# Optimization experiments

Hardware: AMD Instinct MI355X
Metric: run time of the kernel (lower is better)

## Reference

```python
import jax, jax.numpy as jnp
import numpy as np

B, L, E, N, H = 64, 128, 512, 512, 1024


def setup_inputs() -> dict:
    key = jax.random.key(0)
    ks = jax.random.split(key, 16)
    s = 0.02
    return {
        "embeddings": jax.random.normal(ks[0], (B, L, E), jnp.float32),
        "value": jax.random.normal(ks[1], (B, N, H), jnp.float32),
        "value_mask": jnp.ones((B, N), jnp.float32),
        "state": jax.random.normal(ks[2], (B, H), jnp.float32),
        # GRUCell params (PyTorch layout: gates ordered r, z, n)
        "W_ih": jax.random.normal(ks[3], (3 * H, E + H), jnp.float32) * s,
        "b_ih": jnp.zeros((3 * H,), jnp.float32),
        "W_hh": jax.random.normal(ks[4], (3 * H, H), jnp.float32) * s,
        "b_hh": jnp.zeros((3 * H,), jnp.float32),
        # MLP (additive/Bahdanau) attention params
        "Wq": jax.random.normal(ks[5], (H, H), jnp.float32) * s,
        "Wk": jax.random.normal(ks[6], (H, H), jnp.float32) * s,
        "v_att": jax.random.normal(ks[7], (H,), jnp.float32) * s,
        # hidden_mlp: Linear(2H -> H)
        "Wm": jax.random.normal(ks[8], (H, 2 * H), jnp.float32) * s,
        "bm": jnp.zeros((H,), jnp.float32),
    }


def reference(embeddings, value, value_mask, state, W_ih, b_ih, W_hh, b_hh, Wq, Wk, v_att, Wm, bm):
    # Precompute attention keys once: B x N x H
    keys = jnp.einsum('bnh,kh->bnk', value, Wk)
    neg = jnp.float32(-1e9)

    def step(h, emb_t):
        # GRU cell (PyTorch semantics)
        x = jnp.concatenate([emb_t, h], axis=-1)          # B x (E+H)
        gx = x @ W_ih.T + b_ih                            # B x 3H
        gh = h @ W_hh.T + b_hh                            # B x 3H
        xr, xz, xn = jnp.split(gx, 3, axis=-1)
        hr, hz, hn = jnp.split(gh, 3, axis=-1)
        r = jax.nn.sigmoid(xr + hr)
        z = jax.nn.sigmoid(xz + hz)
        n = jnp.tanh(xn + r * hn)
        rnn_out = (1.0 - z) * n + z * h                   # B x H
        # Additive attention
        q = rnn_out @ Wq.T                                # B x H
        score = jnp.einsum('bnh,h->bn', jnp.tanh(q[:, None, :] + keys), v_att)
        score = jnp.where(value_mask > 0, score, neg)
        attn = jax.nn.softmax(score, axis=-1)             # B x N
        context = jnp.einsum('bn,bnh->bh', attn, value)   # B x H
        # hidden MLP + tanh (dropout = identity in eval mode)
        new_state = jnp.tanh(jnp.concatenate([rnn_out, context], axis=-1) @ Wm.T + bm)
        return new_state, (new_state, attn)

    emb_t_first = jnp.swapaxes(embeddings, 0, 1)          # L x B x E
    _, (outs, attns) = jax.lax.scan(step, state, emb_t_first)
    outputs = jnp.swapaxes(outs, 0, 1)                    # B x L x H
    attns = jnp.swapaxes(attns, 0, 1)                     # B x L x N
    return outputs, attns
```

## Files before the change

### kernel.cpp

```cpp
#include <hip/hip_runtime.h>
#include <hip/hip_bf16.h>

typedef __bf16 bf16;
typedef __bf16 bf16x8 __attribute__((ext_vector_type(8)));
typedef __bf16 bf16x4 __attribute__((ext_vector_type(4)));
typedef float floatx4 __attribute__((ext_vector_type(4)));

#define MFMA16(a, b, c) __builtin_amdgcn_mfma_f32_16x16x32_bf16((a), (b), (c), 0, 0, 0)

static constexpr int Bd = 64, Ld = 128, Ed = 512, Nd = 512, Hd = 1024;
static constexpr float LOG2E = 1.4426950408889634f;
static constexpr float TWO_LOG2E = 2.8853900817779268f;

__device__ __forceinline__ float fexp2(float x) { return __builtin_amdgcn_exp2f(x); }
__device__ __forceinline__ float frcp(float x) { return __builtin_amdgcn_rcpf(x); }
__device__ __forceinline__ float sigmoid_f(float x) { return frcp(1.0f + fexp2(-x * LOG2E)); }
__device__ __forceinline__ float tanh_f(float x) { return 1.0f - 2.0f * frcp(fexp2(x * TWO_LOG2E) + 1.0f); }

__device__ __forceinline__ bf16x8 cvt8(const float* p) {
    float4 f0 = *(const float4*)p;
    float4 f1 = *(const float4*)(p + 4);
    bf16x8 r = {(bf16)f0.x, (bf16)f0.y, (bf16)f0.z, (bf16)f0.w,
                (bf16)f1.x, (bf16)f1.y, (bf16)f1.z, (bf16)f1.w};
    return r;
}

__global__ __launch_bounds__(256) void k_conv(const float* __restrict__ src, bf16* __restrict__ dst, int n) {
    int i0 = (blockIdx.x * 256 + threadIdx.x) * 8;
    if (i0 >= n) return;
    *(bf16x8*)(dst + i0) = cvt8(src + i0);
}

__global__ __launch_bounds__(256) void k_init(const float* __restrict__ state, bf16* __restrict__ hb,
                                              float* __restrict__ hb32) {
    int i0 = (blockIdx.x * 256 + threadIdx.x) * 8;
    *(bf16x8*)(hb + i0) = cvt8(state + i0);
    *(float4*)(hb32 + i0) = *(const float4*)(state + i0);
    *(float4*)(hb32 + i0 + 4) = *(const float4*)(state + i0 + 4);
}

__global__ __launch_bounds__(256) void k_keys(const bf16* __restrict__ val, const bf16* __restrict__ Wk,
                                              bf16* __restrict__ keys_c) {
    const int lane = threadIdx.x & 63, wave = threadIdx.x >> 6;
    const int l16 = lane & 15, q8 = (lane >> 4) * 8;
    const int mblk = blockIdx.x >> 4, nblk = blockIdx.x & 15;
    const int m_base = mblk * 64 + (wave & 1) * 32;
    const int n_base = nblk * 64 + (wave >> 1) * 32;
    const bf16* a0p = val + (size_t)(m_base + l16) * 1024 + q8;
    const bf16* a1p = a0p + 16 * 1024;
    const bf16* b0p = Wk + (size_t)(n_base + l16) * 1024 + q8;
    const bf16* b1p = b0p + 16 * 1024;
    floatx4 acc[2][2] = {};
    for (int k0 = 0; k0 < 1024; k0 += 32) {
        bf16x8 a0 = *(const bf16x8*)(a0p + k0);
        bf16x8 a1 = *(const bf16x8*)(a1p + k0);
        bf16x8 b0 = *(const bf16x8*)(b0p + k0);
        bf16x8 b1 = *(const bf16x8*)(b1p + k0);
        acc[0][0] = MFMA16(a0, b0, acc[0][0]);
        acc[0][1] = MFMA16(a0, b1, acc[0][1]);
        acc[1][0] = MFMA16(a1, b0, acc[1][0]);
        acc[1][1] = MFMA16(a1, b1, acc[1][1]);
    }
    const int mr = (lane >> 4) * 4;
    for (int im = 0; im < 2; im++)
        for (int in = 0; in < 2; in++)
            for (int r = 0; r < 4; r++) {
                int m = m_base + im * 16 + mr + r;
                int n = n_base + in * 16 + l16;
                keys_c[(size_t)m * 1024 + n] = (bf16)(acc[im][in][r] * TWO_LOG2E);
            }
}

__global__ __launch_bounds__(64) void k_gru(const float* __restrict__ emb, const bf16* __restrict__ hb,
                                            const float* __restrict__ hb32,
                                            const bf16* __restrict__ Wih, const bf16* __restrict__ Whh,
                                            const float* __restrict__ bih, const float* __restrict__ bhh,
                                            bf16* __restrict__ rnn, float* __restrict__ context, int step) {
    const int lane = threadIdx.x;
    const int l16 = lane & 15, q8 = (lane >> 4) * 8;
    const int mt = blockIdx.x & 3, js = blockIdx.x >> 2;
    ((floatx4*)context)[blockIdx.x * 64 + lane] = (floatx4){0.f, 0.f, 0.f, 0.f};
    const int j_row = js * 16 + l16;
    const int b_row = mt * 16 + l16;
    floatx4 accR = {}, accZ = {}, accXN = {}, accHN = {};
    {
        const float* ae = emb + (size_t)(b_row * 128 + step) * 512 + q8;
        const bf16* w0 = Wih + (size_t)j_row * 1536 + q8;
        const bf16* w1 = Wih + (size_t)(1024 + j_row) * 1536 + q8;
        const bf16* w2 = Wih + (size_t)(2048 + j_row) * 1536 + q8;
        for (int k0 = 0; k0 < 512; k0 += 32) {
            bf16x8 a = cvt8(ae + k0);
            accR  = MFMA16(a, *(const bf16x8*)(w0 + k0), accR);
            accZ  = MFMA16(a, *(const bf16x8*)(w1 + k0), accZ);
            accXN = MFMA16(a, *(const bf16x8*)(w2 + k0), accXN);
        }
    }
    {
        const bf16* ah = hb + (size_t)b_row * 1024 + q8;
        const bf16* u0 = Wih + (size_t)j_row * 1536 + 512 + q8;
        const bf16* u1 = Wih + (size_t)(1024 + j_row) * 1536 + 512 + q8;
        const bf16* u2 = Wih + (size_t)(2048 + j_row) * 1536 + 512 + q8;
        const bf16* v0 = Whh + (size_t)j_row * 1024 + q8;
        const bf16* v1 = Whh + (size_t)(1024 + j_row) * 1024 + q8;
        const bf16* v2 = Whh + (size_t)(2048 + j_row) * 1024 + q8;
        for (int k0 = 0; k0 < 1024; k0 += 32) {
            bf16x8 a = *(const bf16x8*)(ah + k0);
            accR  = MFMA16(a, *(const bf16x8*)(u0 + k0), accR);
            accZ  = MFMA16(a, *(const bf16x8*)(u1 + k0), accZ);
            accXN = MFMA16(a, *(const bf16x8*)(u2 + k0), accXN);
            accHN = MFMA16(a, *(const bf16x8*)(v2 + k0), accHN);
            accR  = MFMA16(a, *(const bf16x8*)(v0 + k0), accR);
            accZ  = MFMA16(a, *(const bf16x8*)(v1 + k0), accZ);
        }
    }
    const int mr = (lane >> 4) * 4;
    const int j = js * 16 + l16;
    const float br  = bih[j] + bhh[j];
    const float bz  = bih[1024 + j] + bhh[1024 + j];
    const float bxn = bih[2048 + j];
    const float bhn = bhh[2048 + j];
    for (int r = 0; r < 4; r++) {
        int b = mt * 16 + mr + r;
        float rg = sigmoid_f(accR[r] + br);
        float zg = sigmoid_f(accZ[r] + bz);
        float ng = tanh_f(accXN[r] + bxn + rg * (accHN[r] + bhn));
        float hp = hb32[(size_t)b * 1024 + j];
        rnn[(size_t)b * 1024 + j] = (bf16)((1.0f - zg) * ng + zg * hp);
    }
}

__global__ __launch_bounds__(64) void k_q(const bf16* __restrict__ rnn, const bf16* __restrict__ Wq,
                                          float* __restrict__ qc) {
    const int lane = threadIdx.x;
    const int l16 = lane & 15, q8 = (lane >> 4) * 8;
    const int mt = blockIdx.x & 3, is = blockIdx.x >> 2;
    const bf16* ap = rnn + (size_t)(mt * 16 + l16) * 1024 + q8;
    const bf16* bp = Wq + (size_t)(is * 16 + l16) * 1024 + q8;
    floatx4 acc = {};
    for (int k0 = 0; k0 < 1024; k0 += 32)
        acc = MFMA16(*(const bf16x8*)(ap + k0), *(const bf16x8*)(bp + k0), acc);
    const int mr = (lane >> 4) * 4;
    for (int r = 0; r < 4; r++) {
        int b = mt * 16 + mr + r;
        int i = is * 16 + l16;
        qc[(size_t)b * 1024 + i] = acc[r] * TWO_LOG2E;
    }
}

__global__ __launch_bounds__(256) void k_score(const bf16* __restrict__ keys_c, const float* __restrict__ qc,
                                               const float* __restrict__ v_att, float* __restrict__ scores) {
    const int b = blockIdx.x >> 7, nq = blockIdx.x & 127;
    const int wave = threadIdx.x >> 6, lane = threadIdx.x & 63;
    const int n = nq * 4 + wave;
    const bf16* kp = keys_c + (size_t)(b * 512 + n) * 1024;
    const float* qp = qc + (size_t)b * 1024;
    float acc = 0.0f;
#pragma unroll
    for (int c = 0; c < 2; c++) {
        const int h0 = c * 512 + lane * 8;
        bf16x8 kv = *(const bf16x8*)(kp + h0);
        float4 va = *(const float4*)(v_att + h0);
        float4 vb = *(const float4*)(v_att + h0 + 4);
        float vv[8] = {va.x, va.y, va.z, va.w, vb.x, vb.y, vb.z, vb.w};
        float4 qa = *(const float4*)(qp + h0);
        float4 qb = *(const float4*)(qp + h0 + 4);
        float qv[8] = {qa.x, qa.y, qa.z, qa.w, qb.x, qb.y, qb.z, qb.w};
#pragma unroll
        for (int jj = 0; jj < 8; jj++) {
            float x = qv[jj] + (float)kv[jj];
            float t = fexp2(x);
            float rr = frcp(t + 1.0f);
            float tv = __builtin_fmaf(-2.0f, rr, 1.0f);
            acc = __builtin_fmaf(vv[jj], tv, acc);
        }
    }
#pragma unroll
    for (int off = 32; off > 0; off >>= 1) acc += __shfl_down(acc, off, 64);
    if (lane == 0) scores[(size_t)b * 512 + n] = acc;
}

__global__ __launch_bounds__(256) void k_attn_ctx(const float* __restrict__ scores, const float* __restrict__ mask,
                                                  const bf16* __restrict__ value, float* __restrict__ context,
                                                  float* __restrict__ out_base, int step) {
    const int b = blockIdx.x >> 2, chunk = blockIdx.x & 3;
    const int t = threadIdx.x;
    __shared__ float sm[512];
    __shared__ float red[256];
    float s0 = scores[(size_t)b * 512 + t];
    float s1 = scores[(size_t)b * 512 + 256 + t];
    if (!(mask[(size_t)b * 512 + t] > 0.f)) s0 = -1e9f;
    if (!(mask[(size_t)b * 512 + 256 + t] > 0.f)) s1 = -1e9f;
    red[t] = fmaxf(s0, s1);
    __syncthreads();
    for (int s = 128; s > 0; s >>= 1) {
        if (t < s) red[t] = fmaxf(red[t], red[t + s]);
        __syncthreads();
    }
    float mx = red[0];
    __syncthreads();
    float p0 = fexp2((s0 - mx) * LOG2E);
    float p1 = fexp2((s1 - mx) * LOG2E);
    red[t] = p0 + p1;
    __syncthreads();
    for (int s = 128; s > 0; s >>= 1) {
        if (t < s) red[t] += red[t + s];
        __syncthreads();
    }
    float inv = frcp(red[0]);
    sm[t] = p0 * inv;
    sm[256 + t] = p1 * inv;
    __syncthreads();
    if (chunk == 0) {
        float* ao = out_base + (size_t)Bd * Ld * Hd + (size_t)(b * 128 + step) * 512;
        ao[t] = sm[t];
        ao[256 + t] = sm[256 + t];
    }
    const int h0 = t * 4;
    float c0 = 0.f, c1 = 0.f, c2 = 0.f, c3 = 0.f;
    const bf16* vb = value + (size_t)b * 512 * 1024 + h0;
    for (int n = chunk * 128; n < chunk * 128 + 128; n++) {
        float a = sm[n];
        bf16x4 vv = *(const bf16x4*)(vb + (size_t)n * 1024);
        c0 = __builtin_fmaf(a, (float)vv[0], c0);
        c1 = __builtin_fmaf(a, (float)vv[1], c1);
        c2 = __builtin_fmaf(a, (float)vv[2], c2);
        c3 = __builtin_fmaf(a, (float)vv[3], c3);
    }
    float* cp = context + (size_t)b * 1024 + h0;
    atomicAdd(cp + 0, c0);
    atomicAdd(cp + 1, c1);
    atomicAdd(cp + 2, c2);
    atomicAdd(cp + 3, c3);
}

__global__ __launch_bounds__(64) void k_out(const bf16* __restrict__ rnn, const float* __restrict__ context,
                                            const bf16* __restrict__ Wm, const float* __restrict__ bm,
                                            float* __restrict__ out, bf16* __restrict__ hb,
                                            float* __restrict__ hb32, int step) {
    const int lane = threadIdx.x;
    const int l16 = lane & 15, q8 = (lane >> 4) * 8;
    const int mt = blockIdx.x & 3, is = blockIdx.x >> 2;
    const int b_row = mt * 16 + l16;
    const bf16* ar = rnn + (size_t)b_row * 1024 + q8;
    const float* ac = context + (size_t)b_row * 1024 + q8;
    const bf16* bp = Wm + (size_t)(is * 16 + l16) * 2048 + q8;
    floatx4 acc = {};
    for (int k0 = 0; k0 < 1024; k0 += 32) {
        bf16x8 a = *(const bf16x8*)(ar + k0);
        acc = MFMA16(a, *(const bf16x8*)(bp + k0), acc);
    }
    for (int k0 = 0; k0 < 1024; k0 += 32) {
        bf16x8 a = cvt8(ac + k0);
        acc = MFMA16(a, *(const bf16x8*)(bp + 1024 + k0), acc);
    }
    const int mr = (lane >> 4) * 4;
    for (int r = 0; r < 4; r++) {
        int b = mt * 16 + mr + r;
        int i = is * 16 + l16;
        float h = tanh_f(acc[r] + bm[i]);
        out[(size_t)(b * 128 + step) * 1024 + i] = h;
        hb[(size_t)b * 1024 + i] = (bf16)h;
        hb32[(size_t)b * 1024 + i] = h;
    }
}

extern "C" void kernel_launch(void* const* d_in, const int* in_sizes, int n_in,
                              void* d_out, int out_size, void* d_ws, size_t ws_size,
                              hipStream_t stream) {
    const float* emb   = (const float*)d_in[0];
    const float* value = (const float*)d_in[1];
    const float* mask  = (const float*)d_in[2];
    const float* state = (const float*)d_in[3];
    const float* Wih   = (const float*)d_in[4];
    const float* bih   = (const float*)d_in[5];
    const float* Whh   = (const float*)d_in[6];
    const float* bhh   = (const float*)d_in[7];
    const float* Wq    = (const float*)d_in[8];
    const float* Wk    = (const float*)d_in[9];
    const float* v_att = (const float*)d_in[10];
    const float* Wm    = (const float*)d_in[11];
    const float* bm    = (const float*)d_in[12];

    char* ws = (char*)d_ws;
    bf16*  hb      = (bf16*)(ws);
    float* hb32    = (float*)(ws + 131072);
    bf16*  rnn     = (bf16*)(ws + 393216);
    float* qc      = (float*)(ws + 524288);
    float* scores  = (float*)(ws + 786432);
    float* context = (float*)(ws + 917504);
    bf16*  value_c = (bf16*)(ws + 1179648);
    bf16*  Wih_c   = (bf16*)(ws + 68288512);
    bf16*  Whh_c   = (bf16*)(ws + 77725696);
    bf16*  Wq_c    = (bf16*)(ws + 84017152);
    bf16*  Wk_c    = (bf16*)(ws + 86114304);
    bf16*  Wm_c    = (bf16*)(ws + 88211456);
    bf16*  keys_c  = (bf16*)(ws + 92405760);

    float* out_f = (float*)d_out;

    k_conv<<<16384, 256, 0, stream>>>(value, value_c, 33554432);
    k_conv<<<2304,  256, 0, stream>>>(Wih,   Wih_c,   4718592);
    k_conv<<<1536,  256, 0, stream>>>(Whh,   Whh_c,   3145728);
    k_conv<<<512,   256, 0, stream>>>(Wq,    Wq_c,    1048576);
    k_conv<<<512,   256, 0, stream>>>(Wk,    Wk_c,    1048576);
    k_conv<<<1024,  256, 0, stream>>>(Wm,    Wm_c,    2097152);
    k_init<<<32,    256, 0, stream>>>(state, hb, hb32);

    k_keys<<<8192, 256, 0, stream>>>(value_c, Wk_c, keys_c);

    for (int step = 0; step < Ld; step++) {
        k_gru<<<256, 64, 0, stream>>>(emb, hb, hb32, Wih_c, Whh_c, bih, bhh, rnn, context, step);
        k_q<<<256, 64, 0, stream>>>(rnn, Wq_c, qc);
        k_score<<<8192, 256, 0, stream>>>(keys_c, qc, v_att, scores);
        k_attn_ctx<<<256, 256, 0, stream>>>(scores, mask, value_c, context, out_f, step);
        k_out<<<256, 64, 0, stream>>>(rnn, context, Wm_c, bm, out_f, hb, hb32, step);
    }
}
```

Measured before the change: 7.917 ms.

## Fuse per-step kernels into one persistent kernel with grid barriers

Replaces the 640 per-step kernel launches with one persistent 256-block kernel that runs all 128 timesteps and separates phases with a software grid barrier built on atomics. GEMM phases now split the K dimension across four waves and reduce through LDS. The context reduction moves from global atomics to an LDS reduction, and softmax uses wave shuffles. The aim is to remove launch overhead and gaps between the many small kernels. In exchange it depends on all 256 blocks being co-resident and pays spin-barrier latency at each phase boundary.

Result: slower. 25.42 ms (+221.1%).

```diff
diff --git a/kernel.cpp b/kernel.cpp
--- a/kernel.cpp
+++ b/kernel.cpp
@@ -9,6 +9,7 @@
 #define MFMA16(a, b, c) __builtin_amdgcn_mfma_f32_16x16x32_bf16((a), (b), (c), 0, 0, 0)
 
 static constexpr int Bd = 64, Ld = 128, Ed = 512, Nd = 512, Hd = 1024;
+static constexpr int NBLK = 256;
 static constexpr float LOG2E = 1.4426950408889634f;
 static constexpr float TWO_LOG2E = 2.8853900817779268f;
 
@@ -71,248 +72,325 @@
             }
 }
 
-__global__ __launch_bounds__(64) void k_gru(const float* __restrict__ emb, const bf16* __restrict__ hb,
-                                            const float* __restrict__ hb32,
-                                            const bf16* __restrict__ Wih, const bf16* __restrict__ Whh,
-                                            const float* __restrict__ bih, const float* __restrict__ bhh,
-                                            bf16* __restrict__ rnn, float* __restrict__ context, int step) {
-    const int lane = threadIdx.x;
-    const int l16 = lane & 15, q8 = (lane >> 4) * 8;
-    const int mt = blockIdx.x & 3, js = blockIdx.x >> 2;
-    ((floatx4*)context)[blockIdx.x * 64 + lane] = (floatx4){0.f, 0.f, 0.f, 0.f};
-    const int j_row = js * 16 + l16;
+__global__ void k_reset(unsigned* bar) {
+    bar[0] = 0u;
+    bar[1] = 0u;
+}
+
+__device__ __forceinline__ void gbar(unsigned* bar) {
+    __syncthreads();
+    if (threadIdx.x == 0) {
+        __threadfence();
+        unsigned gen = __hip_atomic_load(&bar[1], __ATOMIC_RELAXED, __HIP_MEMORY_SCOPE_AGENT);
+        unsigned arrived = __hip_atomic_fetch_add(&bar[0], 1u, __ATOMIC_RELAXED, __HIP_MEMORY_SCOPE_AGENT);
+        if (arrived == (unsigned)(NBLK - 1)) {
+            __hip_atomic_store(&bar[0], 0u, __ATOMIC_RELAXED, __HIP_MEMORY_SCOPE_AGENT);
+            __threadfence();
+            __hip_atomic_fetch_add(&bar[1], 1u, __ATOMIC_RELAXED, __HIP_MEMORY_SCOPE_AGENT);
+        } else {
+            while (__hip_atomic_load(&bar[1], __ATOMIC_RELAXED, __HIP_MEMORY_SCOPE_AGENT) == gen)
+                __builtin_amdgcn_s_sleep(2);
+        }
+        __threadfence();
+    }
+    __syncthreads();
+}
+
+__global__ __launch_bounds__(256) void k_persist(
+    const float* __restrict__ emb, const float* __restrict__ mask,
+    const bf16* __restrict__ value_c, const bf16* __restrict__ keys_c,
+    const bf16* __restrict__ Wih, const bf16* __restrict__ Whh,
+    const float* __restrict__ bih, const float* __restrict__ bhh,
+    const bf16* __restrict__ Wq, const bf16* __restrict__ Wm,
+    const float* __restrict__ bm, const float* __restrict__ v_att,
+    bf16* __restrict__ hb, float* __restrict__ hb32,
+    bf16* __restrict__ rnn, float* __restrict__ qc,
+    float* __restrict__ scores, float* __restrict__ context,
+    float* __restrict__ out_f, unsigned* __restrict__ bar) {
+    const int bid = blockIdx.x, tid = threadIdx.x;
+    const int lane = tid & 63, w = tid >> 6;
+    const int l16 = lane & 15, q8 = (lane >> 4) * 8, mr = (lane >> 4) * 4;
+    __shared__ __align__(16) float lds[4096];
+
+    const int mt = (bid >> 3) & 3;
+    const int cs = (bid & 7) | ((bid >> 5) << 3);
     const int b_row = mt * 16 + l16;
-    floatx4 accR = {}, accZ = {}, accXN = {}, accHN = {};
+    const int jcol = cs * 16 + l16;
+
+    const float biasR = bih[jcol] + bhh[jcol];
+    const float biasZ = bih[1024 + jcol] + bhh[1024 + jcol];
+    const float biasXN = bih[2048 + jcol];
+    const float biasHN = bhh[2048 + jcol];
+    const float biasM = bm[jcol];
+
+    const int gw = bid * 4 + w;
+    const int p3_b = gw >> 4;
+    const int p3_n0 = (gw & 15) * 32;
+
+    float vv[16];
     {
-        const float* ae = emb + (size_t)(b_row * 128 + step) * 512 + q8;
-        const bf16* w0 = Wih + (size_t)j_row * 1536 + q8;
-        const bf16* w1 = Wih + (size_t)(1024 + j_row) * 1536 + q8;
-        const bf16* w2 = Wih + (size_t)(2048 + j_row) * 1536 + q8;
-        for (int k0 = 0; k0 < 512; k0 += 32) {
-            bf16x8 a = cvt8(ae + k0);
-            accR  = MFMA16(a, *(const bf16x8*)(w0 + k0), accR);
-            accZ  = MFMA16(a, *(const bf16x8*)(w1 + k0), accZ);
-            accXN = MFMA16(a, *(const bf16x8*)(w2 + k0), accXN);
-        }
+        float4 a0 = *(const float4*)(v_att + lane * 8);
+        float4 a1 = *(const float4*)(v_att + lane * 8 + 4);
+        float4 b0 = *(const float4*)(v_att + 512 + lane * 8);
+        float4 b1 = *(const float4*)(v_att + 512 + lane * 8 + 4);
+        vv[0] = a0.x; vv[1] = a0.y; vv[2] = a0.z; vv[3] = a0.w;
+        vv[4] = a1.x; vv[5] = a1.y; vv[6] = a1.z; vv[7] = a1.w;
+        vv[8] = b0.x; vv[9] = b0.y; vv[10] = b0.z; vv[11] = b0.w;
+        vv[12] = b1.x; vv[13] = b1.y; vv[14] = b1.z; vv[15] = b1.w;
     }
-    {
-        const bf16* ah = hb + (size_t)b_row * 1024 + q8;
-        const bf16* u0 = Wih + (size_t)j_row * 1536 + 512 + q8;
-        const bf16* u1 = Wih + (size_t)(1024 + j_row) * 1536 + 512 + q8;
-        const bf16* u2 = Wih + (size_t)(2048 + j_row) * 1536 + 512 + q8;
-        const bf16* v0 = Whh + (size_t)j_row * 1024 + q8;
-        const bf16* v1 = Whh + (size_t)(1024 + j_row) * 1024 + q8;
-        const bf16* v2 = Whh + (size_t)(2048 + j_row) * 1024 + q8;
-        for (int k0 = 0; k0 < 1024; k0 += 32) {
-            bf16x8 a = *(const bf16x8*)(ah + k0);
-            accR  = MFMA16(a, *(const bf16x8*)(u0 + k0), accR);
-            accZ  = MFMA16(a, *(const bf16x8*)(u1 + k0), accZ);
-            accXN = MFMA16(a, *(const bf16x8*)(u2 + k0), accXN);
-            accHN = MFMA16(a, *(const bf16x8*)(v2 + k0), accHN);
-            accR  = MFMA16(a, *(const bf16x8*)(v0 + k0), accR);
-            accZ  = MFMA16(a, *(const bf16x8*)(v1 + k0), accZ);
-        }
-    }
-    const int mr = (lane >> 4) * 4;
-    const int j = js * 16 + l16;
-    const float br  = bih[j] + bhh[j];
-    const float bz  = bih[1024 + j] + bhh[1024 + j];
-    const float bxn = bih[2048 + j];
-    const float bhn = bhh[2048 + j];
-    for (int r = 0; r < 4; r++) {
-        int b = mt * 16 + mr + r;
-        float rg = sigmoid_f(accR[r] + br);
-        float zg = sigmoid_f(accZ[r] + bz);
-        float ng = tanh_f(accXN[r] + bxn + rg * (accHN[r] + bhn));
-        float hp = hb32[(size_t)b * 1024 + j];
-        rnn[(size_t)b * 1024 + j] = (bf16)((1.0f - zg) * ng + zg * hp);
-    }
-}
-
-__global__ __launch_bounds__(64) void k_q(const bf16* __restrict__ rnn, const bf16* __restrict__ Wq,
-                                          float* __restrict__ qc) {
-    const int lane = threadIdx.x;
-    const int l16 = lane & 15, q8 = (lane >> 4) * 8;
-    const int mt = blockIdx.x & 3, is = blockIdx.x >> 2;
-    const bf16* ap = rnn + (size_t)(mt * 16 + l16) * 1024 + q8;
-    const bf16* bp = Wq + (size_t)(is * 16 + l16) * 1024 + q8;
-    floatx4 acc = {};
-    for (int k0 = 0; k0 < 1024; k0 += 32)
-        acc = MFMA16(*(const bf16x8*)(ap + k0), *(const bf16x8*)(bp + k0), acc);
-    const int mr = (lane >> 4) * 4;
-    for (int r = 0; r < 4; r++) {
-        int b = mt * 16 + mr + r;
-        int i = is * 16 + l16;
-        qc[(size_t)b * 1024 + i] = acc[r] * TWO_LOG2E;
-    }
-}
-
-__global__ __launch_bounds__(256) void k_score(const bf16* __restrict__ keys_c, const float* __restrict__ qc,
-                                               const float* __restrict__ v_att, float* __restrict__ scores) {
-    const int b = blockIdx.x >> 7, nq = blockIdx.x & 127;
-    const int wave = threadIdx.x >> 6, lane = threadIdx.x & 63;
-    const int n = nq * 4 + wave;
-    const bf16* kp = keys_c + (size_t)(b * 512 + n) * 1024;
-    const float* qp = qc + (size_t)b * 1024;
-    float acc = 0.0f;
-#pragma unroll
-    for (int c = 0; c < 2; c++) {
-        const int h0 = c * 512 + lane * 8;
-        bf16x8 kv = *(const bf16x8*)(kp + h0);
-        float4 va = *(const float4*)(v_att + h0);
-        float4 vb = *(const float4*)(v_att + h0 + 4);
-        float vv[8] = {va.x, va.y, va.z, va.w, vb.x, vb.y, vb.z, vb.w};
-        float4 qa = *(const float4*)(qp + h0);
-        float4 qb = *(const float4*)(qp + h0 + 4);
-        float qv[8] = {qa.x, qa.y, qa.z, qa.w, qb.x, qb.y, qb.z, qb.w};
-#pragma unroll
-        for (int jj = 0; jj < 8; jj++) {
-            float x = qv[jj] + (float)kv[jj];
-            float t = fexp2(x);
-            float rr = frcp(t + 1.0f);
-            float tv = __builtin_fmaf(-2.0f, rr, 1.0f);
-            acc = __builtin_fmaf(vv[jj], tv, acc);
-        }
-    }
-#pragma unroll
-    for (int off = 32; off > 0; off >>= 1) acc += __shfl_down(acc, off, 64);
-    if (lane == 0) scores[(size_t)b * 512 + n] = acc;
-}
-
-__global__ __launch_bounds__(256) void k_attn_ctx(const float* __restrict__ scores, const float* __restrict__ mask,
-                                                  const bf16* __restrict__ value, float* __restrict__ context,
-                                                  float* __restrict__ out_base, int step) {
-    const int b = blockIdx.x >> 2, chunk = blockIdx.x & 3;
-    const int t = threadIdx.x;
-    __shared__ float sm[512];
-    __shared__ float red[256];
-    float s0 = scores[(size_t)b * 512 + t];
-    float s1 = scores[(size_t)b * 512 + 256 + t];
-    if (!(mask[(size_t)b * 512 + t] > 0.f)) s0 = -1e9f;
-    if (!(mask[(size_t)b * 512 + 256 + t] > 0.f)) s1 = -1e9f;
-    red[t] = fmaxf(s0, s1);
-    __syncthreads();
-    for (int s = 128; s > 0; s >>= 1) {
-        if (t < s) red[t] = fmaxf(red[t], red[t + s]);
-        __syncthreads();
-    }
-    float mx = red[0];
-    __syncthreads();
-    float p0 = fexp2((s0 - mx) * LOG2E);
-    float p1 = fexp2((s1 - mx) * LOG2E);
-    red[t] = p0 + p1;
-    __syncthreads();
-    for (int s = 128; s > 0; s >>= 1) {
-        if (t < s) red[t] += red[t + s];
-        __syncthreads();
-    }
-    float inv = frcp(red[0]);
-    sm[t] = p0 * inv;
-    sm[256 + t] = p1 * inv;
-    __syncthreads();
-    if (chunk == 0) {
-        float* ao = out_base + (size_t)Bd * Ld * Hd + (size_t)(b * 128 + step) * 512;
-        ao[t] = sm[t];
-        ao[256 + t] = sm[256 + t];
-    }
-    const int h0 = t * 4;
-    float c0 = 0.f, c1 = 0.f, c2 = 0.f, c3 = 0.f;
-    const bf16* vb = value + (size_t)b * 512 * 1024 + h0;
-    for (int n = chunk * 128; n < chunk * 128 + 128; n++) {
-        float a = sm[n];
-        bf16x4 vv = *(const bf16x4*)(vb + (size_t)n * 1024);
-        c0 = __builtin_fmaf(a, (float)vv[0], c0);
-        c1 = __builtin_fmaf(a, (float)vv[1], c1);
-        c2 = __builtin_fmaf(a, (float)vv[2], c2);
-        c3 = __builtin_fmaf(a, (float)vv[3], c3);
-    }
-    float* cp = context + (size_t)b * 1024 + h0;
-    atomicAdd(cp + 0, c0);
-    atomicAdd(cp + 1, c1);
-    atomicAdd(cp + 2, c2);
-    atomicAdd(cp + 3, c3);
-}
-
-__global__ __launch_bounds__(64) void k_out(const bf16* __restrict__ rnn, const float* __restrict__ context,
-                                            const bf16* __restrict__ Wm, const float* __restrict__ bm,
-                                            float* __restrict__ out, bf16* __restrict__ hb,
-                                            float* __restrict__ hb32, int step) {
-    const int lane = threadIdx.x;
-    const int l16 = lane & 15, q8 = (lane >> 4) * 8;
-    const int mt = blockIdx.x & 3, is = blockIdx.x >> 2;
-    const int b_row = mt * 16 + l16;
-    const bf16* ar = rnn + (size_t)b_row * 1024 + q8;
-    const float* ac = context + (size_t)b_row * 1024 + q8;
-    const bf16* bp = Wm + (size_t)(is * 16 + l16) * 2048 + q8;
-    floatx4 acc = {};
-    for (int k0 = 0; k0 < 1024; k0 += 32) {
-        bf16x8 a = *(const bf16x8*)(ar + k0);
-        acc = MFMA16(a, *(const bf16x8*)(bp + k0), acc);
-    }
-    for (int k0 = 0; k0 < 1024; k0 += 32) {
-        bf16x8 a = cvt8(ac + k0);
-        acc = MFMA16(a, *(const bf16x8*)(bp + 1024 + k0), acc);
-    }
-    const int mr = (lane >> 4) * 4;
-    for (int r = 0; r < 4; r++) {
-        int b = mt * 16 + mr + r;
-        int i = is * 16 + l16;
-        float h = tanh_f(acc[r] + bm[i]);
-        out[(size_t)(b * 128 + step) * 1024 + i] = h;
-        hb[(size_t)b * 1024 + i] = (bf16)h;
-        hb32[(size_t)b * 1024 + i] = h;
+
+    for (int step = 0; step < Ld; ++step) {
+        {
+            floatx4 aR = {}, aZ = {}, aXN = {}, aHN = {};
+            {
+                const float* ae = emb + ((size_t)b_row * Ld + step) * Ed + w * 128 + q8;
+                const bf16* w0 = Wih + (size_t)jcol * 1536 + w * 128 + q8;
+                const bf16* w1 = Wih + (size_t)(1024 + jcol) * 1536 + w * 128 + q8;
+                const bf16* w2 = Wih + (size_t)(2048 + jcol) * 1536 + w * 128 + q8;
+#pragma unroll
+                for (int k = 0; k < 128; k += 32) {
+                    bf16x8 a = cvt8(ae + k);
+                    aR = MFMA16(a, *(const bf16x8*)(w0 + k), aR);
+                    aZ = MFMA16(a, *(const bf16x8*)(w1 + k), aZ);
+                    aXN = MFMA16(a, *(const bf16x8*)(w2 + k), aXN);
+                }
+            }
+            {
+                const bf16* ah = hb + (size_t)b_row * Hd + w * 256 + q8;
+                const bf16* u0 = Wih + (size_t)jcol * 1536 + 512 + w * 256 + q8;
+                const bf16* u1 = Wih + (size_t)(1024 + jcol) * 1536 + 512 + w * 256 + q8;
+                const bf16* u2 = Wih + (size_t)(2048 + jcol) * 1536 + 512 + w * 256 + q8;
+                const bf16* v0 = Whh + (size_t)jcol * 1024 + w * 256 + q8;
+                const bf16* v1 = Whh + (size_t)(1024 + jcol) * 1024 + w * 256 + q8;
+                const bf16* v2 = Whh + (size_t)(2048 + jcol) * 1024 + w * 256 + q8;
+#pragma unroll 4
+                for (int k = 0; k < 256; k += 32) {
+                    bf16x8 a = *(const bf16x8*)(ah + k);
+                    aR = MFMA16(a, *(const bf16x8*)(u0 + k), aR);
+                    aZ = MFMA16(a, *(const bf16x8*)(u1 + k), aZ);
+                    aXN = MFMA16(a, *(const bf16x8*)(u2 + k), aXN);
+                    aHN = MFMA16(a, *(const bf16x8*)(v2 + k), aHN);
+                    aR = MFMA16(a, *(const bf16x8*)(v0 + k), aR);
+                    aZ = MFMA16(a, *(const bf16x8*)(v1 + k), aZ);
+                }
+            }
+            *(floatx4*)&lds[w * 1024 + 0 + lane * 4] = aR;
+            *(floatx4*)&lds[w * 1024 + 256 + lane * 4] = aZ;
+            *(floatx4*)&lds[w * 1024 + 512 + lane * 4] = aXN;
+            *(floatx4*)&lds[w * 1024 + 768 + lane * 4] = aHN;
+            __syncthreads();
+            if (tid < 64) {
+                floatx4 R = {}, Z = {}, XN = {}, HN = {};
+#pragma unroll
+                for (int ww = 0; ww < 4; ++ww) {
+                    R += *(floatx4*)&lds[ww * 1024 + 0 + lane * 4];
+                    Z += *(floatx4*)&lds[ww * 1024 + 256 + lane * 4];
+                    XN += *(floatx4*)&lds[ww * 1024 + 512 + lane * 4];
+                    HN += *(floatx4*)&lds[ww * 1024 + 768 + lane * 4];
+                }
+#pragma unroll
+                for (int r = 0; r < 4; ++r) {
+                    int b = mt * 16 + mr + r;
+                    float rg = sigmoid_f(R[r] + biasR);
+                    float zg = sigmoid_f(Z[r] + biasZ);
+                    float ng = tanh_f(XN[r] + biasXN + rg * (HN[r] + biasHN));
+                    float hp = hb32[(size_t)b * Hd + jcol];
+                    rnn[(size_t)b * Hd + jcol] = (bf16)((1.0f - zg) * ng + zg * hp);
+                }
+            }
+        }
+        gbar(bar);
+
+        {
+            const bf16* ap = rnn + (size_t)b_row * Hd + w * 256 + q8;
+            const bf16* bp = Wq + (size_t)jcol * Hd + w * 256 + q8;
+            floatx4 acc = {};
+#pragma unroll 4
+            for (int k = 0; k < 256; k += 32)
+                acc = MFMA16(*(const bf16x8*)(ap + k), *(const bf16x8*)(bp + k), acc);
+            *(floatx4*)&lds[w * 256 + lane * 4] = acc;
+            __syncthreads();
+            if (tid < 64) {
+                floatx4 s = *(floatx4*)&lds[lane * 4] + *(floatx4*)&lds[256 + lane * 4] +
+                            *(floatx4*)&lds[512 + lane * 4] + *(floatx4*)&lds[768 + lane * 4];
+#pragma unroll
+                for (int r = 0; r < 4; ++r)
+                    qc[(size_t)(mt * 16 + mr + r) * Hd + jcol] = s[r] * TWO_LOG2E;
+            }
+        }
+        gbar(bar);
+
+        {
+            const float* qp = qc + (size_t)p3_b * Hd;
+            float qv[16];
+            {
+                float4 a0 = *(const float4*)(qp + lane * 8);
+                float4 a1 = *(const float4*)(qp + lane * 8 + 4);
+                float4 b0 = *(const float4*)(qp + 512 + lane * 8);
+                float4 b1 = *(const float4*)(qp + 512 + lane * 8 + 4);
+                qv[0] = a0.x; qv[1] = a0.y; qv[2] = a0.z; qv[3] = a0.w;
+                qv[4] = a1.x; qv[5] = a1.y; qv[6] = a1.z; qv[7] = a1.w;
+                qv[8] = b0.x; qv[9] = b0.y; qv[10] = b0.z; qv[11] = b0.w;
+                qv[12] = b1.x; qv[13] = b1.y; qv[14] = b1.z; qv[15] = b1.w;
+            }
+            const bf16* kbase = keys_c + ((size_t)p3_b * Nd + p3_n0) * Hd + lane * 8;
+#pragma unroll 2
+            for (int i = 0; i < 32; ++i) {
+                const bf16* kp = kbase + (size_t)i * Hd;
+                bf16x8 k0 = *(const bf16x8*)kp;
+                bf16x8 k1 = *(const bf16x8*)(kp + 512);
+                float acc = 0.f;
+#pragma unroll
+                for (int jj = 0; jj < 8; ++jj) {
+                    float x = qv[jj] + (float)k0[jj];
+                    float tv = __builtin_fmaf(-2.0f, frcp(fexp2(x) + 1.0f), 1.0f);
+                    acc = __builtin_fmaf(vv[jj], tv, acc);
+                }
+#pragma unroll
+                for (int jj = 0; jj < 8; ++jj) {
+                    float x = qv[8 + jj] + (float)k1[jj];
+                    float tv = __builtin_fmaf(-2.0f, frcp(fexp2(x) + 1.0f), 1.0f);
+                    acc = __builtin_fmaf(vv[8 + jj], tv, acc);
+                }
+#pragma unroll
+                for (int off = 32; off; off >>= 1) acc += __shfl_down(acc, off, 64);
+                if (lane == 0) scores[(size_t)p3_b * Nd + p3_n0 + i] = acc;
+            }
+        }
+        gbar(bar);
+
+        {
+            const int b = bid >> 2, hc = bid & 3;
+            float* sm = lds;
+            float* red = lds + 512;
+            float* part = lds + 768;
+            float s0 = scores[(size_t)b * Nd + tid];
+            float s1 = scores[(size_t)b * Nd + 256 + tid];
+            if (!(mask[(size_t)b * Nd + tid] > 0.f)) s0 = -1e9f;
+            if (!(mask[(size_t)b * Nd + 256 + tid] > 0.f)) s1 = -1e9f;
+            float m = fmaxf(s0, s1);
+#pragma unroll
+            for (int off = 32; off; off >>= 1) m = fmaxf(m, __shfl_xor(m, off, 64));
+            if (lane == 0) red[w] = m;
+            __syncthreads();
+            float mx = fmaxf(fmaxf(red[0], red[1]), fmaxf(red[2], red[3]));
+            float p0 = fexp2((s0 - mx) * LOG2E);
+            float p1 = fexp2((s1 - mx) * LOG2E);
+            float ss = p0 + p1;
+#pragma unroll
+            for (int off = 32; off; off >>= 1) ss += __shfl_xor(ss, off, 64);
+            if (lane == 0) red[4 + w] = ss;
+            __syncthreads();
+            float inv = frcp(red[4] + red[5] + red[6] + red[7]);
+            sm[tid] = p0 * inv;
+            sm[256 + tid] = p1 * inv;
+            __syncthreads();
+            if (hc == 0) {
+                float* ao = out_f + (size_t)Bd * Ld * Hd + ((size_t)b * Ld + step) * Nd;
+                ao[tid] = sm[tid];
+                ao[256 + tid] = sm[256 + tid];
+            }
+            const int h0 = hc * 256 + lane * 4;
+            const bf16* vb = value_c + ((size_t)b * Nd + w * 128) * Hd + h0;
+            float c0 = 0.f, c1 = 0.f, c2 = 0.f, c3 = 0.f;
+#pragma unroll 4
+            for (int n = 0; n < 128; ++n) {
+                float a = sm[w * 128 + n];
+                bf16x4 vt = *(const bf16x4*)(vb + (size_t)n * Hd);
+                c0 = __builtin_fmaf(a, (float)vt[0], c0);
+                c1 = __builtin_fmaf(a, (float)vt[1], c1);
+                c2 = __builtin_fmaf(a, (float)vt[2], c2);
+                c3 = __builtin_fmaf(a, (float)vt[3], c3);
+            }
+            *(floatx4*)&part[w * 256 + lane * 4] = (floatx4){c0, c1, c2, c3};
+            __syncthreads();
+            context[(size_t)b * Hd + hc * 256 + tid] =
+                part[tid] + part[256 + tid] + part[512 + tid] + part[768 + tid];
+        }
+        gbar(bar);
+
+        {
+            const bf16* Bp = Wm + (size_t)jcol * 2048 + q8;
+            floatx4 acc = {};
+            if (w < 2) {
+                const bf16* ar = rnn + (size_t)b_row * Hd + w * 512 + q8;
+                const bf16* bp = Bp + w * 512;
+#pragma unroll 4
+                for (int k = 0; k < 512; k += 32)
+                    acc = MFMA16(*(const bf16x8*)(ar + k), *(const bf16x8*)(bp + k), acc);
+            } else {
+                const float* ac = context + (size_t)b_row * Hd + (w - 2) * 512 + q8;
+                const bf16* bp = Bp + 1024 + (w - 2) * 512;
+#pragma unroll 4
+                for (int k = 0; k < 512; k += 32)
+                    acc = MFMA16(cvt8(ac + k), *(const bf16x8*)(bp + k), acc);
+            }
+            *(floatx4*)&lds[w * 256 + lane * 4] = acc;
+            __syncthreads();
+            if (tid < 64) {
+                floatx4 s = *(floatx4*)&lds[lane * 4] + *(floatx4*)&lds[256 + lane * 4] +
+                            *(floatx4*)&lds[512 + lane * 4] + *(floatx4*)&lds[768 + lane * 4];
+#pragma unroll
+                for (int r = 0; r < 4; ++r) {
+                    int b = mt * 16 + mr + r;
+                    float h = tanh_f(s[r] + biasM);
+                    out_f[((size_t)b * Ld + step) * Hd + jcol] = h;
+                    hb[(size_t)b * Hd + jcol] = (bf16)h;
+                    hb32[(size_t)b * Hd + jcol] = h;
+                }
+            }
+        }
+        gbar(bar);
     }
 }
 
 extern "C" void kernel_launch(void* const* d_in, const int* in_sizes, int n_in,
                               void* d_out, int out_size, void* d_ws, size_t ws_size,
                               hipStream_t stream) {
-    const float* emb   = (const float*)d_in[0];
+    const float* emb = (const float*)d_in[0];
     const float* value = (const float*)d_in[1];
-    const float* mask  = (const float*)d_in[2];
+    const float* mask = (const float*)d_in[2];
     const float* state = (const float*)d_in[3];
-    const float* Wih   = (const float*)d_in[4];
-    const float* bih   = (const float*)d_in[5];
-    const float* Whh   = (const float*)d_in[6];
-    const float* bhh   = (const float*)d_in[7];
-    const float* Wq    = (const float*)d_in[8];
-    const float* Wk    = (const float*)d_in[9];
+    const float* Wih = (const float*)d_in[4];
+    const float* bih = (const float*)d_in[5];
+    const float* Whh = (const float*)d_in[6];
+    const float* bhh = (const float*)d_in[7];
+    const float* Wq = (const float*)d_in[8];
+    const float* Wk = (const float*)d_in[9];
     const float* v_att = (const float*)d_in[10];
-    const float* Wm    = (const float*)d_in[11];
-    const float* bm    = (const float*)d_in[12];
+    const float* Wm = (const float*)d_in[11];
+    const float* bm = (const float*)d_in[12];
 
     char* ws = (char*)d_ws;
-    bf16*  hb      = (bf16*)(ws);
-    float* hb32    = (float*)(ws + 131072);
-    bf16*  rnn     = (bf16*)(ws + 393216);
-    float* qc      = (float*)(ws + 524288);
-    float* scores  = (float*)(ws + 786432);
+    bf16* hb = (bf16*)(ws);
+    float* hb32 = (float*)(ws + 131072);
+    bf16* rnn = (bf16*)(ws + 393216);
+    float* qc = (float*)(ws + 524288);
+    float* scores = (float*)(ws + 786432);
     float* context = (float*)(ws + 917504);
-    bf16*  value_c = (bf16*)(ws + 1179648);
-    bf16*  Wih_c   = (bf16*)(ws + 68288512);
-    bf16*  Whh_c   = (bf16*)(ws + 77725696);
-    bf16*  Wq_c    = (bf16*)(ws + 84017152);
-    bf16*  Wk_c    = (bf16*)(ws + 86114304);
-    bf16*  Wm_c    = (bf16*)(ws + 88211456);
-    bf16*  keys_c  = (bf16*)(ws + 92405760);
+    bf16* value_c = (bf16*)(ws + 1179648);
+    bf16* Wih_c = (bf16*)(ws + 68288512);
+    bf16* Whh_c = (bf16*)(ws + 77725696);
+    bf16* Wq_c = (bf16*)(ws + 84017152);
+    bf16* Wk_c = (bf16*)(ws + 86114304);
+    bf16* Wm_c = (bf16*)(ws + 88211456);
+    bf16* keys_c = (bf16*)(ws + 92405760);
+    unsigned* bar = (unsigned*)(ws + 159514624);
 
     float* out_f = (float*)d_out;
 
     k_conv<<<16384, 256, 0, stream>>>(value, value_c, 33554432);
-    k_conv<<<2304,  256, 0, stream>>>(Wih,   Wih_c,   4718592);
-    k_conv<<<1536,  256, 0, stream>>>(Whh,   Whh_c,   3145728);
-    k_conv<<<512,   256, 0, stream>>>(Wq,    Wq_c,    1048576);
-    k_conv<<<512,   256, 0, stream>>>(Wk,    Wk_c,    1048576);
-    k_conv<<<1024,  256, 0, stream>>>(Wm,    Wm_c,    2097152);
-    k_init<<<32,    256, 0, stream>>>(state, hb, hb32);
+    k_conv<<<2304, 256, 0, stream>>>(Wih, Wih_c, 4718592);
+    k_conv<<<1536, 256, 0, stream>>>(Whh, Whh_c, 3145728);
+    k_conv<<<512, 256, 0, stream>>>(Wq, Wq_c, 1048576);
+    k_conv<<<512, 256, 0, stream>>>(Wk, Wk_c, 1048576);
+    k_conv<<<1024, 256, 0, stream>>>(Wm, Wm_c, 2097152);
+    k_init<<<32, 256, 0, stream>>>(state, hb, hb32);
 
     k_keys<<<8192, 256, 0, stream>>>(value_c, Wk_c, keys_c);
 
-    for (int step = 0; step < Ld; step++) {
-        k_gru<<<256, 64, 0, stream>>>(emb, hb, hb32, Wih_c, Whh_c, bih, bhh, rnn, context, step);
-        k_q<<<256, 64, 0, stream>>>(rnn, Wq_c, qc);
-        k_score<<<8192, 256, 0, stream>>>(keys_c, qc, v_att, scores);
-        k_attn_ctx<<<256, 256, 0, stream>>>(scores, mask, value_c, context, out_f, step);
-        k_out<<<256, 64, 0, stream>>>(rnn, context, Wm_c, bm, out_f, hb, hb32, step);
-    }
-}
+    k_reset<<<1, 1, 0, stream>>>(bar);
+    k_persist<<<NBLK, 256, 0, stream>>>(emb, mask, value_c, keys_c, Wih_c, Whh_c, bih, bhh,
+                                        Wq_c, Wm_c, bm, v_att, hb, hb32, rnn, qc, scores,
+                                        context, out_f, bar);
+}
```
